# Performance work log

Measured on AMD Instinct MI355X. Metric: run time of the kernel, lower is better.

## Reference

```python
import jax, jax.numpy as jnp
import numpy as np

HID = 1024   # utter_hidden * 2
UD = 512     # user_dim
B = 16384


def setup_inputs() -> dict:
    key = jax.random.key(0)
    ks = jax.random.split(key, 15)
    sx = 1.0 / np.sqrt(HID)
    sh = 1.0 / np.sqrt(UD)
    inp = {
        'encoder_hidden': jax.random.normal(ks[0], (B, HID), jnp.float32),
        'spk_vectors': jax.random.normal(ks[1], (B, UD), jnp.float32),
        'adr_vectors': jax.random.normal(ks[2], (B, UD), jnp.float32),
    }
    # torch Linear weights are [out, in]; bias=False everywhere
    names_x = ['WA_xr', 'WA_xp', 'WA_xz', 'WA_xh']
    names_h = ['WA_hr', 'WA_hp', 'WA_hz', 'WA_hh']
    names_v = ['VA_hr', 'VA_hp', 'VA_hz', 'VA_hh']
    i = 3
    for n in names_x:
        inp[n] = jax.random.uniform(ks[i], (UD, HID), jnp.float32, -sx, sx); i += 1
    for n in names_h + names_v:
        inp[n] = jax.random.uniform(ks[i], (UD, UD), jnp.float32, -sh, sh); i += 1
    return inp


def reference(encoder_hidden, spk_vectors, adr_vectors,
              WA_xr, WA_xp, WA_xz, WA_xh,
              WA_hr, WA_hp, WA_hz, WA_hh,
              VA_hr, VA_hp, VA_hz, VA_hh):
    def lin(x, W):  # torch nn.Linear (bias=False): x @ W.T
        return x @ W.T
    r_t = jax.nn.sigmoid(lin(encoder_hidden, WA_xr) + lin(spk_vectors, WA_hr) + lin(adr_vectors, VA_hr))
    p_t = jax.nn.sigmoid(lin(encoder_hidden, WA_xp) + lin(spk_vectors, WA_hp) + lin(adr_vectors, VA_hp))
    z_t = jax.nn.sigmoid(lin(encoder_hidden, WA_xz) + lin(spk_vectors, WA_hz) + lin(adr_vectors, VA_hz))
    h_tilde = jnp.tanh(lin(encoder_hidden, WA_xh) + lin(r_t * spk_vectors, WA_hh) + lin(p_t * adr_vectors, VA_hh))
    return (1.0 - z_t) * spk_vectors + z_t * h_tilde
```

## Files before the change

### kernel.cpp

```cpp
#include <hip/hip_runtime.h>
#include <hip/hip_bf16.h>
#include <stdint.h>


typedef short  short8  __attribute__((ext_vector_type(8)));
typedef unsigned short ushort8 __attribute__((ext_vector_type(8)));
typedef float  f32x4   __attribute__((ext_vector_type(4)));

static constexpr int Bn  = 16384;

__device__ __forceinline__ unsigned short f2bf(float x) {
  union { float f; unsigned u; } v; v.f = x;
  unsigned r = v.u + 0x7fffu + ((v.u >> 16) & 1u);
  return (unsigned short)(r >> 16);
}
__device__ __forceinline__ float bf2f(unsigned short h) {
  union { unsigned u; float f; } v; v.u = ((unsigned)h) << 16; return v.f;
}
__device__ __forceinline__ float sigm(float x) { return 1.0f / (1.0f + __expf(-x)); }
__device__ __forceinline__ float tanh_fast(float x) {
  return 2.0f / (1.0f + __expf(-2.0f * x)) - 1.0f;
}

__device__ __forceinline__ void gload_lds16(const void* g, void* l) {
  __builtin_amdgcn_global_load_lds((const __attribute__((address_space(1))) void*)g,
                                   (__attribute__((address_space(3))) void*)l,
                                   16, 0, 0);
}

__global__ __launch_bounds__(256) void pack_w1(
    const float* __restrict__ xr, const float* __restrict__ xp,
    const float* __restrict__ xz, const float* __restrict__ xh,
    const float* __restrict__ hr, const float* __restrict__ hp, const float* __restrict__ hz,
    const float* __restrict__ vr, const float* __restrict__ vp, const float* __restrict__ vz,
    unsigned short* __restrict__ W1)
{
  int idx = blockIdx.x * 256 + threadIdx.x;
  int n  = idx >> 8;
  int k8 = (idx & 255) << 3;
  int g = n >> 9, j = n & 511;
  const float* src = nullptr;
  if (k8 < 1024) {
    const float* x = (g == 0) ? xr : (g == 1) ? xp : (g == 2) ? xz : xh;
    src = x + (size_t)j * 1024 + k8;
  } else if (k8 < 1536) {
    if (g < 3) { const float* h = (g == 0) ? hr : (g == 1) ? hp : hz; src = h + (size_t)j * 512 + (k8 - 1024); }
  } else {
    if (g < 3) { const float* v = (g == 0) ? vr : (g == 1) ? vp : vz; src = v + (size_t)j * 512 + (k8 - 1536); }
  }
  ushort8 o;
  if (src) { for (int i = 0; i < 8; i++) o[i] = f2bf(src[i]); }
  else     { for (int i = 0; i < 8; i++) o[i] = 0; }
  *(ushort8*)&W1[(size_t)n * 2048 + k8] = o;
}

__global__ __launch_bounds__(256) void pack_w2(
    const float* __restrict__ hh, const float* __restrict__ vh,
    unsigned short* __restrict__ W2)
{
  int idx = blockIdx.x * 256 + threadIdx.x;
  int n  = idx >> 7;
  int k8 = (idx & 127) << 3;
  const float* src = (k8 < 512) ? hh + (size_t)n * 512 + k8
                                : vh + (size_t)n * 512 + (k8 - 512);
  ushort8 o;
  for (int i = 0; i < 8; i++) o[i] = f2bf(src[i]);
  *(ushort8*)&W2[(size_t)n * 1024 + k8] = o;
}

__global__ __launch_bounds__(256) void pack_u(
    const float* __restrict__ X, const float* __restrict__ S, const float* __restrict__ A,
    unsigned short* __restrict__ U)
{
  int idx = blockIdx.x * 256 + threadIdx.x;
  int b  = idx >> 8;
  int c8 = (idx & 255) << 3;
  const float* src = (c8 < 1024) ? X + (size_t)b * 1024 + c8
                   : (c8 < 1536) ? S + (size_t)b * 512 + (c8 - 1024)
                                 : A + (size_t)b * 512 + (c8 - 1536);
  f32x4 lo = *(const f32x4*)src;
  f32x4 hi = *(const f32x4*)(src + 4);
  ushort8 o;
  o[0] = f2bf(lo[0]); o[1] = f2bf(lo[1]); o[2] = f2bf(lo[2]); o[3] = f2bf(lo[3]);
  o[4] = f2bf(hi[0]); o[5] = f2bf(hi[1]); o[6] = f2bf(hi[2]); o[7] = f2bf(hi[3]);
  *(ushort8*)&U[(size_t)b * 2048 + c8] = o;
}

__global__ __launch_bounds__(512, 1) void gemm256_epi1(
    const unsigned short* __restrict__ Amat,
    const unsigned short* __restrict__ Bmat,
    const int K,
    unsigned short* __restrict__ U2, unsigned short* __restrict__ Zp,
    unsigned short* __restrict__ XHp)
{
  extern __shared__ char lds[];

  const int tid  = threadIdx.x;
  const int lane = tid & 63, wave = tid >> 6;
  const int wm = wave >> 2, wn = wave & 3;
  const int fr = lane & 15, fq = lane >> 4;

  const int k_xcd = blockIdx.x & 7;
  const int i_loc = (int)blockIdx.x >> 3;
  const int n0 = (i_loc & 7) * 256;
  const int m0 = (k_xcd * 8 + (i_loc >> 3)) * 256;

  const int Keff = (n0 >= 1536) ? 1024 : K;
  const int NT   = Keff >> 6;

  const int srow  = tid >> 3;
  const int sslot = (tid & 7) ^ (srow & 7);
  const unsigned short* gA = Amat + (size_t)(m0 + srow) * K + sslot * 8;
  const unsigned short* gB = Bmat + (size_t)(n0 + srow) * K + sslot * 8;
  const size_t K64 = (size_t)64 * K;

  int swz[2];
  swz[0] = ((fq    ) ^ (fr & 7)) << 4;
  swz[1] = ((fq + 4) ^ (fr & 7)) << 4;
  const int aoff = wm * 16384 + fr * 128;
  const int boff = 32768 + wn * 8192 + fr * 128;

  f32x4 acc[8][4] = {};

  auto STAGE = [&](int buf, int tile) {
    const int bufo = buf << 16;
#pragma unroll
    for (int j = 0; j < 4; j++) {
      gload_lds16(gA + (size_t)j * K64 + (tile << 6), lds + bufo + tid * 16 + j * 8192);
      gload_lds16(gB + (size_t)j * K64 + (tile << 6), lds + bufo + 32768 + tid * 16 + j * 8192);
    }
  };
  auto COMPUTE = [&](int buf) {
    const int bufo = buf << 16;
    short8 b[4][2];
#pragma unroll
    for (int ni = 0; ni < 4; ni++)
#pragma unroll
      for (int ks = 0; ks < 2; ks++)
        b[ni][ks] = *(const short8*)(lds + bufo + boff + ni * 2048 + swz[ks]);
#pragma unroll
    for (int c = 0; c < 4; c++) {
      short8 a[2][2];
#pragma unroll
      for (int i = 0; i < 2; i++)
#pragma unroll
        for (int ks = 0; ks < 2; ks++)
          a[i][ks] = *(const short8*)(lds + bufo + aoff + (c * 2 + i) * 2048 + swz[ks]);
#pragma unroll
      for (int i = 0; i < 2; i++)
#pragma unroll
        for (int ni = 0; ni < 4; ni++)
#pragma unroll
          for (int ks = 0; ks < 2; ks++)
            acc[c * 2 + i][ni] = __builtin_amdgcn_mfma_f32_16x16x32_bf16(
                a[i][ks], b[ni][ks], acc[c * 2 + i][ni], 0, 0, 0);
    }
  };

  STAGE(0, 0);
  __syncthreads();

  int cur = 0;
  for (int t = 0; t < NT - 1; ++t) {
    STAGE(cur ^ 1, t + 1);
    COMPUTE(cur);
    __syncthreads();
    cur ^= 1;
  }
  COMPUTE(cur);

#pragma unroll
  for (int mi = 0; mi < 8; mi++) {
#pragma unroll
    for (int ni = 0; ni < 4; ni++) {
      const int ncol = n0 + wn * 64 + ni * 16 + fr;
      const int gate = ncol >> 9, j = ncol & 511;
#pragma unroll
      for (int jj = 0; jj < 4; jj++) {
        const size_t rb = (size_t)(m0 + wm * 128 + mi * 16 + fq * 4 + jj);
        const float v = acc[mi][ni][jj];
        if (gate == 0) {
          const float s = bf2f(Amat[rb * 2048 + 1024 + j]);
          U2[rb * 1024 + j] = f2bf(sigm(v) * s);
        } else if (gate == 1) {
          const float a = bf2f(Amat[rb * 2048 + 1536 + j]);
          U2[rb * 1024 + 512 + j] = f2bf(sigm(v) * a);
        } else if (gate == 2) {
          Zp[rb * 512 + j]  = f2bf(v);
        } else {
          XHp[rb * 512 + j] = f2bf(v);
        }
      }
    }
  }
}

template<int NPAN>
__global__ __launch_bounds__(256) void gemm_bt2(
    const unsigned short* __restrict__ Amat,
    const unsigned short* __restrict__ Bmat,
    const int K,
    const float* __restrict__ Sv,
    const unsigned short* __restrict__ Zp,
    const unsigned short* __restrict__ XHp, float* __restrict__ Out)
{
  constexpr int BK = 32;
  __shared__ __align__(16) unsigned short sA[128 * BK];
  __shared__ __align__(16) unsigned short sB[128 * BK];

  const int tid  = threadIdx.x;
  const int lane = tid & 63;
  const int wave = tid >> 6;
  const int wr = wave >> 1, wc = wave & 1;

  const int k_xcd = blockIdx.x & 7;
  const int i_loc = (int)blockIdx.x >> 3;
  const int n_loc = i_loc % NPAN;
  const int m_loc = i_loc / NPAN;
  const int mpan_per_xcd = (int)(gridDim.x >> 3) / NPAN;
  const int m0 = (k_xcd * mpan_per_xcd + m_loc) * 128;
  const int n0 = n_loc * 128;

  const int q = tid >> 2, r = tid & 3;
  const unsigned short* gA = Amat + (size_t)(m0 + q) * K + r * 8;
  const unsigned short* gB = Bmat + (size_t)(n0 + q) * K + r * 8;

  f32x4 acc[4][4] = {};
  const int fr = lane & 15, fq = lane >> 4;

  for (int kt = 0; kt < K; kt += BK) {
    gload_lds16(gA + kt,                  &sA[tid * 8]);
    gload_lds16(gA + kt + (size_t)64 * K, &sA[2048 + tid * 8]);
    gload_lds16(gB + kt,                  &sB[tid * 8]);
    gload_lds16(gB + kt + (size_t)64 * K, &sB[2048 + tid * 8]);
    __syncthreads();

    short8 a[4], b[4];
#pragma unroll
    for (int mt = 0; mt < 4; mt++)
      a[mt] = *(const short8*)&sA[(wr * 64 + mt * 16 + fr) * 32 + fq * 8];
#pragma unroll
    for (int nt = 0; nt < 4; nt++)
      b[nt] = *(const short8*)&sB[(wc * 64 + nt * 16 + fr) * 32 + fq * 8];
#pragma unroll
    for (int mt = 0; mt < 4; mt++)
#pragma unroll
      for (int nt = 0; nt < 4; nt++)
        acc[mt][nt] = __builtin_amdgcn_mfma_f32_16x16x32_bf16(a[mt], b[nt], acc[mt][nt], 0, 0, 0);
    __syncthreads();
  }

#pragma unroll
  for (int mt = 0; mt < 4; mt++) {
#pragma unroll
    for (int nt = 0; nt < 4; nt++) {
      const int ncol = n0 + wc * 64 + nt * 16 + fr;
#pragma unroll
      for (int jj = 0; jj < 4; jj++) {
        const size_t rb = (size_t)(m0 + wr * 64 + mt * 16 + fq * 4 + jj);
        const size_t o = rb * 512 + ncol;
        const float z = sigm(bf2f(Zp[o]));
        const float h = tanh_fast(bf2f(XHp[o]) + acc[mt][nt][jj]);
        Out[o] = (1.0f - z) * Sv[o] + z * h;
      }
    }
  }
}


extern "C" void kernel_launch(void* const* d_in, const int* in_sizes, int n_in,
                              void* d_out, int out_size, void* d_ws, size_t ws_size,
                              hipStream_t stream) {
  const float* X   = (const float*)d_in[0];
  const float* S   = (const float*)d_in[1];
  const float* A   = (const float*)d_in[2];
  const float* Wxr = (const float*)d_in[3];
  const float* Wxp = (const float*)d_in[4];
  const float* Wxz = (const float*)d_in[5];
  const float* Wxh = (const float*)d_in[6];
  const float* Whr = (const float*)d_in[7];
  const float* Whp = (const float*)d_in[8];
  const float* Whz = (const float*)d_in[9];
  const float* Whh = (const float*)d_in[10];
  const float* Vhr = (const float*)d_in[11];
  const float* Vhp = (const float*)d_in[12];
  const float* Vhz = (const float*)d_in[13];
  const float* Vhh = (const float*)d_in[14];

  char* ws = (char*)d_ws;
  size_t off = 0;
  auto alloc = [&](size_t bytes) -> void* {
    void* p = ws + off;
    off += (bytes + 255) & ~(size_t)255;
    return p;
  };
  unsigned short* W1 = (unsigned short*)alloc((size_t)2048 * 2048 * 2);
  unsigned short* W2 = (unsigned short*)alloc((size_t)512 * 1024 * 2);
  unsigned short* U  = (unsigned short*)alloc((size_t)Bn * 2048 * 2);
  unsigned short* U2 = (unsigned short*)alloc((size_t)Bn * 1024 * 2);
  unsigned short* Zp = (unsigned short*)alloc((size_t)Bn * 512 * 2);
  unsigned short* XH = (unsigned short*)alloc((size_t)Bn * 512 * 2);

  pack_w1<<<2048, 256, 0, stream>>>(Wxr, Wxp, Wxz, Wxh, Whr, Whp, Whz, Vhr, Vhp, Vhz, W1);
  pack_w2<<<256, 256, 0, stream>>>(Whh, Vhh, W2);
  pack_u <<<Bn, 256, 0, stream>>>(X, S, A, U);

  (void)hipFuncSetAttribute((const void*)gemm256_epi1,
                            hipFuncAttributeMaxDynamicSharedMemorySize, 131072);

  gemm256_epi1<<<512, 512, 131072, stream>>>(U, W1, 2048, U2, Zp, XH);

  gemm_bt2<4><<<512, 256, 0, stream>>>(U2, W2, 1024, S, Zp, XH, (float*)d_out);
}
```

Baseline: 296.3 us.

## Merge pack kernels and retile second GEMM with swizzled double-buffered LDS

Folds the input-pack and W1-pack kernels into one launch. Replaces the second GEMM with a 256x128 tile, 512-thread kernel that uses swizzled, double-buffered LDS staging with BK=64 instead of a single-buffered BK=32 loop. The epilogue now reads the spk value from the packed bf16 U buffer instead of the fp32 input, which cuts bandwidth slightly at a small precision cost. The grid shrinks to 256 blocks, which may underfill the 256 CUs if occupancy is one block per CU.

After: 277.5 us. 6.3% less time.

```diff
diff --git a/kernel.cpp b/kernel.cpp
--- a/kernel.cpp
+++ b/kernel.cpp
@@ -28,33 +28,51 @@
                                    16, 0, 0);
 }
 
-__global__ __launch_bounds__(256) void pack_w1(
+__global__ __launch_bounds__(256) void pack_all(
+    const float* __restrict__ X, const float* __restrict__ S, const float* __restrict__ A,
     const float* __restrict__ xr, const float* __restrict__ xp,
     const float* __restrict__ xz, const float* __restrict__ xh,
     const float* __restrict__ hr, const float* __restrict__ hp, const float* __restrict__ hz,
     const float* __restrict__ vr, const float* __restrict__ vp, const float* __restrict__ vz,
-    unsigned short* __restrict__ W1)
+    unsigned short* __restrict__ U, unsigned short* __restrict__ W1)
 {
-  int idx = blockIdx.x * 256 + threadIdx.x;
-  int n  = idx >> 8;
-  int k8 = (idx & 255) << 3;
-  int g = n >> 9, j = n & 511;
-  const float* src = nullptr;
-  if (k8 < 1024) {
-    const float* x = (g == 0) ? xr : (g == 1) ? xp : (g == 2) ? xz : xh;
-    src = x + (size_t)j * 1024 + k8;
-  } else if (k8 < 1536) {
-    if (g < 3) { const float* h = (g == 0) ? hr : (g == 1) ? hp : hz; src = h + (size_t)j * 512 + (k8 - 1024); }
+  const int bid = blockIdx.x;
+  const int tid = threadIdx.x;
+  if (bid < 16384) {
+    int idx = bid * 256 + tid;
+    int b  = idx >> 8;
+    int c8 = (idx & 255) << 3;
+    const float* src = (c8 < 1024) ? X + (size_t)b * 1024 + c8
+                     : (c8 < 1536) ? S + (size_t)b * 512 + (c8 - 1024)
+                                   : A + (size_t)b * 512 + (c8 - 1536);
+    f32x4 lo = *(const f32x4*)src;
+    f32x4 hi = *(const f32x4*)(src + 4);
+    ushort8 o;
+    o[0] = f2bf(lo[0]); o[1] = f2bf(lo[1]); o[2] = f2bf(lo[2]); o[3] = f2bf(lo[3]);
+    o[4] = f2bf(hi[0]); o[5] = f2bf(hi[1]); o[6] = f2bf(hi[2]); o[7] = f2bf(hi[3]);
+    *(ushort8*)&U[(size_t)b * 2048 + c8] = o;
   } else {
-    if (g < 3) { const float* v = (g == 0) ? vr : (g == 1) ? vp : vz; src = v + (size_t)j * 512 + (k8 - 1536); }
-  }
-  ushort8 o;
-  if (src) { for (int i = 0; i < 8; i++) o[i] = f2bf(src[i]); }
-  else     { for (int i = 0; i < 8; i++) o[i] = 0; }
-  *(ushort8*)&W1[(size_t)n * 2048 + k8] = o;
-}
-
-__global__ __launch_bounds__(256) void pack_w2(
+    int idx = (bid - 16384) * 256 + tid;
+    int n  = idx >> 8;
+    int k8 = (idx & 255) << 3;
+    int g = n >> 9, j = n & 511;
+    const float* src = nullptr;
+    if (k8 < 1024) {
+      const float* x = (g == 0) ? xr : (g == 1) ? xp : (g == 2) ? xz : xh;
+      src = x + (size_t)j * 1024 + k8;
+    } else if (k8 < 1536) {
+      if (g < 3) { const float* h = (g == 0) ? hr : (g == 1) ? hp : hz; src = h + (size_t)j * 512 + (k8 - 1024); }
+    } else {
+      if (g < 3) { const float* v = (g == 0) ? vr : (g == 1) ? vp : vz; src = v + (size_t)j * 512 + (k8 - 1536); }
+    }
+    ushort8 o;
+    if (src) { for (int i = 0; i < 8; i++) o[i] = f2bf(src[i]); }
+    else     { for (int i = 0; i < 8; i++) o[i] = 0; }
+    *(ushort8*)&W1[(size_t)n * 2048 + k8] = o;
+  }
+}
+
+__global__ __launch_bounds__(256) void pack_w2k(
     const float* __restrict__ hh, const float* __restrict__ vh,
     unsigned short* __restrict__ W2)
 {
@@ -68,24 +86,6 @@
   *(ushort8*)&W2[(size_t)n * 1024 + k8] = o;
 }
 
-__global__ __launch_bounds__(256) void pack_u(
-    const float* __restrict__ X, const float* __restrict__ S, const float* __restrict__ A,
-    unsigned short* __restrict__ U)
-{
-  int idx = blockIdx.x * 256 + threadIdx.x;
-  int b  = idx >> 8;
-  int c8 = (idx & 255) << 3;
-  const float* src = (c8 < 1024) ? X + (size_t)b * 1024 + c8
-                   : (c8 < 1536) ? S + (size_t)b * 512 + (c8 - 1024)
-                                 : A + (size_t)b * 512 + (c8 - 1536);
-  f32x4 lo = *(const f32x4*)src;
-  f32x4 hi = *(const f32x4*)(src + 4);
-  ushort8 o;
-  o[0] = f2bf(lo[0]); o[1] = f2bf(lo[1]); o[2] = f2bf(lo[2]); o[3] = f2bf(lo[3]);
-  o[4] = f2bf(hi[0]); o[5] = f2bf(hi[1]); o[6] = f2bf(hi[2]); o[7] = f2bf(hi[3]);
-  *(ushort8*)&U[(size_t)b * 2048 + c8] = o;
-}
-
 __global__ __launch_bounds__(512, 1) void gemm256_epi1(
     const unsigned short* __restrict__ Amat,
     const unsigned short* __restrict__ Bmat,
@@ -183,8 +183,8 @@
           const float s = bf2f(Amat[rb * 2048 + 1024 + j]);
           U2[rb * 1024 + j] = f2bf(sigm(v) * s);
         } else if (gate == 1) {
-          const float a = bf2f(Amat[rb * 2048 + 1536 + j]);
-          U2[rb * 1024 + 512 + j] = f2bf(sigm(v) * a);
+          const float a2 = bf2f(Amat[rb * 2048 + 1536 + j]);
+          U2[rb * 1024 + 512 + j] = f2bf(sigm(v) * a2);
         } else if (gate == 2) {
           Zp[rb * 512 + j]  = f2bf(v);
         } else {
@@ -195,73 +195,101 @@
   }
 }
 
-template<int NPAN>
-__global__ __launch_bounds__(256) void gemm_bt2(
-    const unsigned short* __restrict__ Amat,
-    const unsigned short* __restrict__ Bmat,
-    const int K,
-    const float* __restrict__ Sv,
+__global__ __launch_bounds__(512, 1) void gemm2_fin(
+    const unsigned short* __restrict__ U2,
+    const unsigned short* __restrict__ W2,
+    const unsigned short* __restrict__ Uu,
     const unsigned short* __restrict__ Zp,
     const unsigned short* __restrict__ XHp, float* __restrict__ Out)
 {
-  constexpr int BK = 32;
-  __shared__ __align__(16) unsigned short sA[128 * BK];
-  __shared__ __align__(16) unsigned short sB[128 * BK];
+  extern __shared__ char lds[];
+  constexpr int K = 1024, NT = K >> 6;
 
   const int tid  = threadIdx.x;
-  const int lane = tid & 63;
-  const int wave = tid >> 6;
-  const int wr = wave >> 1, wc = wave & 1;
+  const int lane = tid & 63, wave = tid >> 6;
+  const int wm = wave >> 1, wn = wave & 1;
+  const int fr = lane & 15, fq = lane >> 4;
 
   const int k_xcd = blockIdx.x & 7;
   const int i_loc = (int)blockIdx.x >> 3;
-  const int n_loc = i_loc % NPAN;
-  const int m_loc = i_loc / NPAN;
-  const int mpan_per_xcd = (int)(gridDim.x >> 3) / NPAN;
-  const int m0 = (k_xcd * mpan_per_xcd + m_loc) * 128;
-  const int n0 = n_loc * 128;
-
-  const int q = tid >> 2, r = tid & 3;
-  const unsigned short* gA = Amat + (size_t)(m0 + q) * K + r * 8;
-  const unsigned short* gB = Bmat + (size_t)(n0 + q) * K + r * 8;
+  const int n0 = (i_loc & 3) * 128;
+  const int m0 = (k_xcd * 8 + (i_loc >> 2)) * 256;
+
+  const int srow  = tid >> 3;
+  const int sslot = (tid & 7) ^ (srow & 7);
+  const unsigned short* gA = U2 + (size_t)(m0 + srow) * K + sslot * 8;
+  const unsigned short* gB = W2 + (size_t)(n0 + srow) * K + sslot * 8;
+  const size_t K64 = (size_t)64 * K;
+
+  int swz[2];
+  swz[0] = ((fq    ) ^ (fr & 7)) << 4;
+  swz[1] = ((fq + 4) ^ (fr & 7)) << 4;
+  const int aoff = wm * 8192 + fr * 128;
+  const int boff = 32768 + wn * 8192 + fr * 128;
 
   f32x4 acc[4][4] = {};
-  const int fr = lane & 15, fq = lane >> 4;
-
-  for (int kt = 0; kt < K; kt += BK) {
-    gload_lds16(gA + kt,                  &sA[tid * 8]);
-    gload_lds16(gA + kt + (size_t)64 * K, &sA[2048 + tid * 8]);
-    gload_lds16(gB + kt,                  &sB[tid * 8]);
-    gload_lds16(gB + kt + (size_t)64 * K, &sB[2048 + tid * 8]);
+
+  auto STAGE = [&](int buf, int tile) {
+    const int bufo = buf * 49152;
+#pragma unroll
+    for (int j = 0; j < 4; j++)
+      gload_lds16(gA + (size_t)j * K64 + (tile << 6), lds + bufo + tid * 16 + j * 8192);
+#pragma unroll
+    for (int j = 0; j < 2; j++)
+      gload_lds16(gB + (size_t)j * K64 + (tile << 6), lds + bufo + 32768 + tid * 16 + j * 8192);
+  };
+  auto COMPUTE = [&](int buf) {
+    const int bufo = buf * 49152;
+    short8 b[4][2];
+#pragma unroll
+    for (int ni = 0; ni < 4; ni++)
+#pragma unroll
+      for (int ks = 0; ks < 2; ks++)
+        b[ni][ks] = *(const short8*)(lds + bufo + boff + ni * 2048 + swz[ks]);
+#pragma unroll
+    for (int c = 0; c < 2; c++) {
+      short8 a[2][2];
+#pragma unroll
+      for (int i = 0; i < 2; i++)
+#pragma unroll
+        for (int ks = 0; ks < 2; ks++)
+          a[i][ks] = *(const short8*)(lds + bufo + aoff + (c * 2 + i) * 2048 + swz[ks]);
+#pragma unroll
+      for (int i = 0; i < 2; i++)
+#pragma unroll
+        for (int ni = 0; ni < 4; ni++)
+#pragma unroll
+          for (int ks = 0; ks < 2; ks++)
+            acc[c * 2 + i][ni] = __builtin_amdgcn_mfma_f32_16x16x32_bf16(
+                a[i][ks], b[ni][ks], acc[c * 2 + i][ni], 0, 0, 0);
+    }
+  };
+
+  STAGE(0, 0);
+  __syncthreads();
+
+  int cur = 0;
+  for (int t = 0; t < NT - 1; ++t) {
+    STAGE(cur ^ 1, t + 1);
+    COMPUTE(cur);
     __syncthreads();
-
-    short8 a[4], b[4];
-#pragma unroll
-    for (int mt = 0; mt < 4; mt++)
-      a[mt] = *(const short8*)&sA[(wr * 64 + mt * 16 + fr) * 32 + fq * 8];
-#pragma unroll
-    for (int nt = 0; nt < 4; nt++)
-      b[nt] = *(const short8*)&sB[(wc * 64 + nt * 16 + fr) * 32 + fq * 8];
-#pragma unroll
-    for (int mt = 0; mt < 4; mt++)
-#pragma unroll
-      for (int nt = 0; nt < 4; nt++)
-        acc[mt][nt] = __builtin_amdgcn_mfma_f32_16x16x32_bf16(a[mt], b[nt], acc[mt][nt], 0, 0, 0);
-    __syncthreads();
-  }
+    cur ^= 1;
+  }
+  COMPUTE(cur);
 
 #pragma unroll
   for (int mt = 0; mt < 4; mt++) {
 #pragma unroll
     for (int nt = 0; nt < 4; nt++) {
-      const int ncol = n0 + wc * 64 + nt * 16 + fr;
+      const int ncol = n0 + wn * 64 + nt * 16 + fr;
 #pragma unroll
       for (int jj = 0; jj < 4; jj++) {
-        const size_t rb = (size_t)(m0 + wr * 64 + mt * 16 + fq * 4 + jj);
+        const size_t rb = (size_t)(m0 + wm * 64 + mt * 16 + fq * 4 + jj);
         const size_t o = rb * 512 + ncol;
         const float z = sigm(bf2f(Zp[o]));
         const float h = tanh_fast(bf2f(XHp[o]) + acc[mt][nt][jj]);
-        Out[o] = (1.0f - z) * Sv[o] + z * h;
+        const float s = bf2f(Uu[rb * 2048 + 1024 + ncol]);
+        Out[o] = (1.0f - z) * s + z * h;
       }
     }
   }
@@ -301,14 +329,16 @@
   unsigned short* Zp = (unsigned short*)alloc((size_t)Bn * 512 * 2);
   unsigned short* XH = (unsigned short*)alloc((size_t)Bn * 512 * 2);
 
-  pack_w1<<<2048, 256, 0, stream>>>(Wxr, Wxp, Wxz, Wxh, Whr, Whp, Whz, Vhr, Vhp, Vhz, W1);
-  pack_w2<<<256, 256, 0, stream>>>(Whh, Vhh, W2);
-  pack_u <<<Bn, 256, 0, stream>>>(X, S, A, U);
+  pack_all<<<16384 + 2048, 256, 0, stream>>>(
+      X, S, A, Wxr, Wxp, Wxz, Wxh, Whr, Whp, Whz, Vhr, Vhp, Vhz, U, W1);
+  pack_w2k<<<256, 256, 0, stream>>>(Whh, Vhh, W2);
 
   (void)hipFuncSetAttribute((const void*)gemm256_epi1,
                             hipFuncAttributeMaxDynamicSharedMemorySize, 131072);
+  (void)hipFuncSetAttribute((const void*)gemm2_fin,
+                            hipFuncAttributeMaxDynamicSharedMemorySize, 98304);
 
   gemm256_epi1<<<512, 512, 131072, stream>>>(U, W1, 2048, U2, Zp, XH);
 
-  gemm_bt2<4><<<512, 256, 0, stream>>>(U2, W2, 1024, S, Zp, XH, (float*)d_out);
-}
+  gemm2_fin<<<256, 512, 98304, stream>>>(U2, W2, U, Zp, XH, (float*)d_out);
+}
```
